# Kernel tuning notes

Hardware: AMD Instinct MI355X
Metric: run time of the kernel (lower is better)

## Reference

```python
import math
import jax, jax.numpy as jnp
import numpy as np

N = 100000      # nodes
E = 800000      # edges (before self loops)
D_IN = 128      # dim_node
D_H = 64        # dim_hidden
N_CLS = 40      # num_classes
L = 4           # num_layers
ALPHA = 0.1
THETA = 0.5


def setup_inputs() -> dict:
    key = jax.random.key(0)
    ks = jax.random.split(key, 7)
    x = jax.random.normal(ks[0], (N, D_IN), dtype=jnp.float32)
    edge_index = jax.random.randint(ks[1], (2, E), 0, N, dtype=jnp.int64)
    fc0_w = jax.random.normal(ks[2], (D_IN, D_H), dtype=jnp.float32) / math.sqrt(D_IN)
    fc0_b = jnp.zeros((D_H,), dtype=jnp.float32)
    fc1_w = jax.random.normal(ks[3], (D_H, N_CLS), dtype=jnp.float32) / math.sqrt(D_H)
    fc1_b = jnp.zeros((N_CLS,), dtype=jnp.float32)
    conv_w = jax.random.normal(ks[4], (L, D_H, D_H), dtype=jnp.float32) / math.sqrt(D_H)
    return {"x": x, "edge_index": edge_index, "fc0_w": fc0_w, "fc0_b": fc0_b,
            "fc1_w": fc1_w, "fc1_b": fc1_b, "conv_w": conv_w}


def reference(x, edge_index, fc0_w, fc0_b, fc1_w, fc1_b, conv_w):
    # gcn_norm with add_self_loops=True, improved=False (fill_value=1)
    self_idx = jnp.arange(N, dtype=edge_index.dtype)
    row = jnp.concatenate([edge_index[0], self_idx])   # source
    col = jnp.concatenate([edge_index[1], self_idx])   # target
    w = jnp.ones((E + N,), dtype=x.dtype)
    deg = jax.ops.segment_sum(w, col, num_segments=N)
    dinv = jnp.where(deg > 0, jax.lax.rsqrt(deg), 0.0)
    norm = dinv[row] * w * dinv[col]                   # [E+N]

    def prop(h):
        # gather + edge-weight scale + scatter-add (GCNII propagate)
        return jax.ops.segment_sum(norm[:, None] * h[row], col, num_segments=N)

    # fc0 + relu (dropout is identity in eval)
    h = jax.nn.relu(x @ fc0_w + fc0_b)
    # first conv: x_0 is None -> just propagate, then relu
    h = jax.nn.relu(prop(h))
    x0 = h
    for i in range(1, L):
        beta = math.log(THETA / (i + 1) + 1.0)
        m = prop(h)
        m = (1.0 - ALPHA) * m + ALPHA * x0
        # addmm(m, m, W1, beta=1-beta, alpha=beta)
        h = jax.nn.relu((1.0 - beta) * m + beta * (m @ conv_w[i]))
    return h @ fc1_w + fc1_b
```

## Files before the change

### kernel.cpp

```cpp
#include <hip/hip_runtime.h>
#include <hip/hip_fp16.h>

#define N_NODES 100000
#define N_EDGES 800000
#define N_BUCKET 391
#define L_HIST (N_BUCKET * 256)

__device__ inline float4 f4zero() { return make_float4(0.f, 0.f, 0.f, 0.f); }

__device__ inline unsigned pack2u(float a, float b) {
    union { unsigned u; __half2 h; } r; r.h = __floats2half2_rn(a, b); return r.u;
}
__device__ inline float2 unpack2f(unsigned u) {
    union { unsigned uu; __half2 h; } d; d.uu = u; return __half22float2(d.h);
}

typedef _Float16 hf2 __attribute__((ext_vector_type(2)));
__device__ inline float fdot2(unsigned a, unsigned b, float c) {
#if __has_builtin(__builtin_amdgcn_fdot2)
    union { unsigned u; hf2 h; } ua, ub; ua.u = a; ub.u = b;
    return __builtin_amdgcn_fdot2(ua.h, ub.h, c, false);
#else
    float2 fa = unpack2f(a), fb = unpack2f(b);
    return fmaf(fa.x, fb.x, fmaf(fa.y, fb.y, c));
#endif
}

__device__ inline uint4 pack8(const float f[8]) {
    uint4 u;
    u.x = pack2u(f[0], f[1]); u.y = pack2u(f[2], f[3]);
    u.z = pack2u(f[4], f[5]); u.w = pack2u(f[6], f[7]);
    return u;
}
__device__ inline void unpack8(uint4 u, float f[8]) {
    float2 t;
    t = unpack2f(u.x); f[0] = t.x; f[1] = t.y;
    t = unpack2f(u.y); f[2] = t.x; f[3] = t.y;
    t = unpack2f(u.z); f[4] = t.x; f[5] = t.y;
    t = unpack2f(u.w); f[6] = t.x; f[7] = t.y;
}


__global__ __launch_bounds__(256) void k_hist(const int* __restrict__ col, int* __restrict__ histT) {
    __shared__ int hist[N_BUCKET];
    int b = blockIdx.x, t = threadIdx.x;
    for (int i = t; i < N_BUCKET; i += 256) hist[i] = 0;
    __syncthreads();
    const int base = b * 3125;
    for (int i = t; i < 3125; i += 256) atomicAdd(&hist[col[base + i] >> 8], 1);
    __syncthreads();
    for (int d = t; d < N_BUCKET; d += 256) histT[d * 256 + b] = hist[d];
}

__global__ __launch_bounds__(256) void k_scanA(const int* __restrict__ in, int* __restrict__ out,
                                               int* __restrict__ bsum, int L) {
    __shared__ int sh[256];
    int t = threadIdx.x, b = blockIdx.x;
    int base = b * 1024 + t * 4;
    int c0 = 0, c1 = 0, c2 = 0, c3 = 0;
    if (base + 3 < L) {
        int4 v = *reinterpret_cast<const int4*>(in + base);
        c0 = v.x; c1 = v.y; c2 = v.z; c3 = v.w;
    } else {
        if (base + 0 < L) c0 = in[base + 0];
        if (base + 1 < L) c1 = in[base + 1];
        if (base + 2 < L) c2 = in[base + 2];
    }
    int s = c0 + c1 + c2 + c3;
    sh[t] = s;
    __syncthreads();
    for (int off = 1; off < 256; off <<= 1) {
        int add = (t >= off) ? sh[t - off] : 0;
        __syncthreads();
        sh[t] += add;
        __syncthreads();
    }
    int excl = sh[t] - s;
    if (t == 255) bsum[b] = sh[t];
    int p = excl;
    if (base + 0 < L) out[base + 0] = p; p += c0;
    if (base + 1 < L) out[base + 1] = p; p += c1;
    if (base + 2 < L) out[base + 2] = p; p += c2;
    if (base + 3 < L) out[base + 3] = p;
}

__global__ __launch_bounds__(128) void k_scanB(int* __restrict__ bsum, int nb) {
    __shared__ int sh[128];
    int t = threadIdx.x;
    int v = (t < nb) ? bsum[t] : 0;
    sh[t] = v;
    __syncthreads();
    for (int off = 1; off < 128; off <<= 1) {
        int add = (t >= off) ? sh[t - off] : 0;
        __syncthreads();
        sh[t] += add;
        __syncthreads();
    }
    if (t < nb) bsum[t] = sh[t] - v;
}

__global__ __launch_bounds__(256) void k_scanC(int* __restrict__ out, const int* __restrict__ bsum, int L) {
    int t = threadIdx.x, b = blockIdx.x;
    int off = bsum[b];
    int base = b * 1024 + t * 4;
#pragma unroll
    for (int j = 0; j < 4; ++j)
        if (base + j < L) out[base + j] += off;
}

__global__ __launch_bounds__(256) void k_scatter1(const int* __restrict__ row, const int* __restrict__ col,
                                                  const int* __restrict__ hoff, unsigned* __restrict__ tmp) {
    __shared__ int lcnt[N_BUCKET];
    int b = blockIdx.x, t = threadIdx.x;
    for (int d = t; d < N_BUCKET; d += 256) lcnt[d] = hoff[d * 256 + b];
    __syncthreads();
    const int base = b * 3125;
    for (int i = t; i < 3125; i += 256) {
        int c = col[base + i];
        int r = row[base + i];
        int p = atomicAdd(&lcnt[c >> 8], 1);
        tmp[p] = ((unsigned)(c & 255) << 17) | (unsigned)r;
    }
}

__global__ __launch_bounds__(256) void k_bucket(const unsigned* __restrict__ tmp, const int* __restrict__ hoff,
                                                int* __restrict__ starts, int* __restrict__ csr,
                                                float* __restrict__ dinv, float* __restrict__ rsq) {
    __shared__ int hist[256], sh[256], cur[256];
    int d = blockIdx.x, t = threadIdx.x;
    int s0 = hoff[d * 256];
    int s1 = (d < N_BUCKET - 1) ? hoff[(d + 1) * 256] : N_EDGES;
    int len = s1 - s0;
    hist[t] = 0;
    __syncthreads();
    for (int i = t; i < len; i += 256) atomicAdd(&hist[tmp[s0 + i] >> 17], 1);
    __syncthreads();
    int h = hist[t];
    sh[t] = h;
    __syncthreads();
    for (int off = 1; off < 256; off <<= 1) {
        int add = (t >= off) ? sh[t - off] : 0;
        __syncthreads();
        sh[t] += add;
        __syncthreads();
    }
    int excl = sh[t] - h;
    int colg = d * 256 + t;
    if (colg < N_NODES) {
        starts[colg] = s0 + excl;
        dinv[colg] = rsqrtf((float)h + 1.f);
        rsq[colg]  = sqrtf((float)h + 1.f);
    }
    if (d == N_BUCKET - 1 && t == 0) starts[N_NODES] = N_EDGES;
    cur[t] = s0 + excl;
    __syncthreads();
    for (int i = t; i < len; i += 256) {
        unsigned e = tmp[s0 + i];
        int p = atomicAdd(&cur[e >> 17], 1);
        csr[p] = (int)(e & 0x1FFFFu);
    }
}

__global__ __launch_bounds__(256) void k_wcvt(const float* __restrict__ conv_w, const float* __restrict__ fc1_w,
                                              const float* __restrict__ fc0_w,
                                              unsigned* __restrict__ wh, unsigned* __restrict__ w1h,
                                              unsigned* __restrict__ w0h) {
    int i = blockIdx.x * 256 + threadIdx.x;
    if (i < 3 * 2048) {
        int layer = i >> 11, rem = i & 2047, kp = rem >> 6, c = rem & 63;
        const float* wsrc = conv_w + (size_t)(layer + 1) * 4096;
        wh[i] = pack2u(wsrc[(2 * kp) * 64 + c], wsrc[(2 * kp + 1) * 64 + c]);
        return;
    }
    int j = i - 3 * 2048;
    if (j < 1280) {
        int kp = j / 40, c = j - kp * 40;
        w1h[j] = pack2u(fc1_w[(2 * kp) * 40 + c], fc1_w[(2 * kp + 1) * 40 + c]);
        return;
    }
    int t = j - 1280;
    if (t < 4096) {
        int kp = t >> 6, c = t & 63;
        w0h[t] = pack2u(fc0_w[(2 * kp) * 64 + c], fc0_w[(2 * kp + 1) * 64 + c]);
    }
}

__global__ __launch_bounds__(256, 4) void k_fc0(const float* __restrict__ x, const unsigned* __restrict__ w0h,
                                                const float* __restrict__ bias, const float* __restrict__ dinv,
                                                uint2* __restrict__ out) {
    __shared__ unsigned wsh[64 * 64];
    __shared__ unsigned xs2[64 * 65];
    const float4* x4 = reinterpret_cast<const float4*>(x);
    int tid = threadIdx.x;
    int base = blockIdx.x * 64;
#pragma unroll
    for (int i = 0; i < 4; ++i)
        reinterpret_cast<uint4*>(wsh)[tid + 256 * i] = reinterpret_cast<const uint4*>(w0h)[tid + 256 * i];
#pragma unroll
    for (int j = 0; j < 8; ++j) {
        int f = tid + 256 * j;
        int ln = f >> 5, c = f & 31;
        float4 v = (base + ln < N_NODES) ? x4[(size_t)(base + ln) * 32 + c] : f4zero();
        xs2[ln * 65 + 2 * c]     = pack2u(v.x, v.y);
        xs2[ln * 65 + 2 * c + 1] = pack2u(v.z, v.w);
    }
    __syncthreads();
    int q = tid & 15, lbase = (tid >> 4) * 4;
    float4 bv = reinterpret_cast<const float4*>(bias)[q];
    float a[4][4];
#pragma unroll
    for (int n = 0; n < 4; ++n) { a[n][0] = bv.x; a[n][1] = bv.y; a[n][2] = bv.z; a[n][3] = bv.w; }
#pragma unroll 4
    for (int kp = 0; kp < 64; ++kp) {
        unsigned xh0 = xs2[(lbase + 0) * 65 + kp];
        unsigned xh1 = xs2[(lbase + 1) * 65 + kp];
        unsigned xh2 = xs2[(lbase + 2) * 65 + kp];
        unsigned xh3 = xs2[(lbase + 3) * 65 + kp];
        uint4 wv = *reinterpret_cast<const uint4*>(&wsh[kp * 64 + q * 4]);
        a[0][0] = fdot2(xh0, wv.x, a[0][0]); a[0][1] = fdot2(xh0, wv.y, a[0][1]);
        a[0][2] = fdot2(xh0, wv.z, a[0][2]); a[0][3] = fdot2(xh0, wv.w, a[0][3]);
        a[1][0] = fdot2(xh1, wv.x, a[1][0]); a[1][1] = fdot2(xh1, wv.y, a[1][1]);
        a[1][2] = fdot2(xh1, wv.z, a[1][2]); a[1][3] = fdot2(xh1, wv.w, a[1][3]);
        a[2][0] = fdot2(xh2, wv.x, a[2][0]); a[2][1] = fdot2(xh2, wv.y, a[2][1]);
        a[2][2] = fdot2(xh2, wv.z, a[2][2]); a[2][3] = fdot2(xh2, wv.w, a[2][3]);
        a[3][0] = fdot2(xh3, wv.x, a[3][0]); a[3][1] = fdot2(xh3, wv.y, a[3][1]);
        a[3][2] = fdot2(xh3, wv.z, a[3][2]); a[3][3] = fdot2(xh3, wv.w, a[3][3]);
    }
#pragma unroll
    for (int n = 0; n < 4; ++n) {
        int nn = base + lbase + n;
        if (nn < N_NODES) {
            float dc = dinv[nn];
            float r0 = dc * fmaxf(a[n][0], 0.f), r1 = dc * fmaxf(a[n][1], 0.f);
            float r2 = dc * fmaxf(a[n][2], 0.f), r3 = dc * fmaxf(a[n][3], 0.f);
            uint2 u; u.x = pack2u(r0, r1); u.y = pack2u(r2, r3);
            out[(size_t)nn * 16 + q] = u;
        }
    }
}

__device__ __forceinline__ void gather8h(const uint4* __restrict__ hp, const int* __restrict__ csr,
                                         int s, int e, int q, __half2 acc2[4]) {
    if (s >= e) return;
    int l = e - 1;
    int idx[8];
#pragma unroll
    for (int j = 0; j < 8; ++j) idx[j] = csr[min(s + j, l)];
    for (int p = s; p < e; p += 8) {
        uint4 d[8];
        unsigned msk[8];
#pragma unroll
        for (int j = 0; j < 8; ++j) {
            d[j] = hp[(size_t)idx[j] * 8 + q];
            msk[j] = (p + j <= l) ? 0x3C003C00u : 0u;
        }
        if (p + 8 < e) {
#pragma unroll
            for (int j = 0; j < 8; ++j) idx[j] = csr[min(p + 8 + j, l)];
        }
#pragma unroll
        for (int j = 0; j < 8; ++j) {
            __half2 w2 = *reinterpret_cast<__half2*>(&msk[j]);
            const __half2* h2 = reinterpret_cast<const __half2*>(&d[j]);
            acc2[0] = __hfma2(w2, h2[0], acc2[0]);
            acc2[1] = __hfma2(w2, h2[1], acc2[1]);
            acc2[2] = __hfma2(w2, h2[2], acc2[2]);
            acc2[3] = __hfma2(w2, h2[3], acc2[3]);
        }
    }
}

__global__ __launch_bounds__(256, 6) void k_prop0(const uint4* __restrict__ hp, uint4* __restrict__ x0p,
                                                  const float* __restrict__ dinv,
                                                  const int* __restrict__ starts, const int* __restrict__ csr) {
    int t = blockIdx.x * 256 + threadIdx.x;
    int node = t >> 3, q = t & 7;
    uint4 self = hp[(size_t)node * 8 + q];
    __half2 acc2[4];
    const __half2* sh2 = reinterpret_cast<const __half2*>(&self);
#pragma unroll
    for (int k = 0; k < 4; ++k) acc2[k] = sh2[k];
    gather8h(hp, csr, starts[node], starts[node + 1], q, acc2);
    float dc = dinv[node];
    float accf[8];
    unpack8(*reinterpret_cast<uint4*>(acc2), accf);
    float o[8];
#pragma unroll
    for (int k = 0; k < 8; ++k) o[k] = dc * fmaxf(dc * accf[k], 0.f);
    x0p[(size_t)node * 8 + q] = pack8(o);
}

template <bool FINAL>
__global__ __launch_bounds__(256, 6) void k_propconv(
    const uint4* __restrict__ hp_in, const uint4* __restrict__ x0p,
    const float* __restrict__ dinv, const float* __restrict__ rsq,
    const int* __restrict__ starts, const int* __restrict__ csr,
    const unsigned* __restrict__ wh, float beta,
    const unsigned* __restrict__ w1h, const float* __restrict__ b1,
    void* __restrict__ out) {
    __shared__ unsigned ws2[32 * 64];
    __shared__ unsigned ws12[FINAL ? 32 * 40 : 1];

    int tid = threadIdx.x;
    int nl = tid >> 3, q = tid & 7;
    int node = blockIdx.x * 32 + nl;

    reinterpret_cast<uint4*>(ws2)[tid]       = reinterpret_cast<const uint4*>(wh)[tid];
    reinterpret_cast<uint4*>(ws2)[tid + 256] = reinterpret_cast<const uint4*>(wh)[tid + 256];
    if constexpr (FINAL) {
        reinterpret_cast<uint4*>(ws12)[tid < 320 ? tid : 0] = reinterpret_cast<const uint4*>(w1h)[tid < 320 ? tid : 0];
        if (tid < 64) reinterpret_cast<uint4*>(ws12)[tid + 256] = reinterpret_cast<const uint4*>(w1h)[tid + 256];
    }

    uint4 self = hp_in[(size_t)node * 8 + q];
    __half2 acc2[4];
    const __half2* sh2 = reinterpret_cast<const __half2*>(&self);
#pragma unroll
    for (int k = 0; k < 4; ++k) acc2[k] = sh2[k];
    gather8h(hp_in, csr, starts[node], starts[node + 1], q, acc2);

    float dc = dinv[node];
    float rs = rsq[node];
    float accf[8], xq[8];
    unpack8(*reinterpret_cast<uint4*>(acc2), accf);
    unpack8(x0p[(size_t)node * 8 + q], xq);
    float m[8];
#pragma unroll
    for (int k = 0; k < 8; ++k) m[k] = 0.9f * dc * accf[k] + 0.1f * rs * xq[k];
    unsigned mh[4];
#pragma unroll
    for (int t = 0; t < 4; ++t) mh[t] = pack2u(m[2 * t], m[2 * t + 1]);

    __syncthreads();

    float a[8] = {0.f, 0.f, 0.f, 0.f, 0.f, 0.f, 0.f, 0.f};
#pragma unroll
    for (int src = 0; src < 8; ++src) {
        unsigned mm[4];
#pragma unroll
        for (int t = 0; t < 4; ++t) mm[t] = (unsigned)__shfl((int)mh[t], src, 8);
#pragma unroll
        for (int t = 0; t < 4; ++t) {
            int kp = src * 4 + t;
            const uint4* wr = reinterpret_cast<const uint4*>(&ws2[kp * 64 + q * 8]);
            uint4 w0 = wr[0], w1 = wr[1];
            a[0] = fdot2(mm[t], w0.x, a[0]); a[1] = fdot2(mm[t], w0.y, a[1]);
            a[2] = fdot2(mm[t], w0.z, a[2]); a[3] = fdot2(mm[t], w0.w, a[3]);
            a[4] = fdot2(mm[t], w1.x, a[4]); a[5] = fdot2(mm[t], w1.y, a[5]);
            a[6] = fdot2(mm[t], w1.z, a[6]); a[7] = fdot2(mm[t], w1.w, a[7]);
        }
    }
    float omb = 1.f - beta;
    float r[8];
#pragma unroll
    for (int k = 0; k < 8; ++k) r[k] = fmaxf(fmaf(omb, m[k], beta * a[k]), 0.f);

    if constexpr (!FINAL) {
        float o[8];
#pragma unroll
        for (int k = 0; k < 8; ++k) o[k] = dc * r[k];
        reinterpret_cast<uint4*>(out)[(size_t)node * 8 + q] = pack8(o);
    } else {
        unsigned rh[4];
#pragma unroll
        for (int t = 0; t < 4; ++t) rh[t] = pack2u(r[2 * t], r[2 * t + 1]);
        float acc1[5];
#pragma unroll
        for (int j = 0; j < 5; ++j) acc1[j] = b1[q * 5 + j];
#pragma unroll
        for (int src = 0; src < 8; ++src) {
            unsigned rm[4];
#pragma unroll
            for (int t = 0; t < 4; ++t) rm[t] = (unsigned)__shfl((int)rh[t], src, 8);
#pragma unroll
            for (int t = 0; t < 4; ++t) {
                int kp = src * 4 + t;
                const unsigned* wr = &ws12[kp * 40 + q * 5];
#pragma unroll
                for (int j = 0; j < 5; ++j) acc1[j] = fdot2(rm[t], wr[j], acc1[j]);
            }
        }
        float* o = reinterpret_cast<float*>(out) + (size_t)node * 40 + q * 5;
#pragma unroll
        for (int j = 0; j < 5; ++j) o[j] = acc1[j];
    }
}


extern "C" void kernel_launch(void* const* d_in, const int* in_sizes, int n_in,
                              void* d_out, int out_size, void* d_ws, size_t ws_size,
                              hipStream_t stream) {
    const float* x      = (const float*)d_in[0];
    const int*   ei     = (const int*)d_in[1];
    const float* fc0_w  = (const float*)d_in[2];
    const float* fc0_b  = (const float*)d_in[3];
    const float* fc1_w  = (const float*)d_in[4];
    const float* fc1_b  = (const float*)d_in[5];
    const float* conv_w = (const float*)d_in[6];
    const int* row = ei;
    const int* col = ei + N_EDGES;

    char* ws = (char*)d_ws;
    size_t off = 0;
    auto alloc = [&](size_t bytes) -> void* {
        void* p = ws + off;
        off += (bytes + 255) & ~(size_t)255;
        return p;
    };
    float*    dinv   = (float*)alloc((size_t)N_NODES * 4);
    float*    rsq    = (float*)alloc((size_t)N_NODES * 4);
    int*      starts = (int*)alloc((size_t)(N_NODES + 1) * 4);
    int*      histT  = (int*)alloc((size_t)L_HIST * 4);
    int*      hoff   = (int*)alloc((size_t)L_HIST * 4);
    int*      bsum   = (int*)alloc(128 * 4);
    unsigned* tmp    = (unsigned*)alloc((size_t)N_EDGES * 4);
    int*      csr    = (int*)alloc((size_t)N_EDGES * 4);
    unsigned* wh     = (unsigned*)alloc(3 * 2048 * 4);
    unsigned* w1h    = (unsigned*)alloc(1280 * 4);
    unsigned* w0h    = (unsigned*)alloc(4096 * 4);
    uint4*    hp0    = (uint4*)alloc((size_t)N_NODES * 128);
    uint4*    x0p    = (uint4*)alloc((size_t)N_NODES * 128);
    uint4*    hpA    = (uint4*)alloc((size_t)N_NODES * 128);
    uint4*    hpB    = (uint4*)alloc((size_t)N_NODES * 128);
    if (off > ws_size) return;

    const int NBH = (L_HIST + 1023) / 1024;
    const int GMM = (N_NODES + 63) / 64;
    const int GP  = (N_NODES * 8) / 256;
    const int GPC = N_NODES / 32;

    k_wcvt<<<45, 256, 0, stream>>>(conv_w, fc1_w, fc0_w, wh, w1h, w0h);
    k_hist<<<256, 256, 0, stream>>>(col, histT);
    k_scanA<<<NBH, 256, 0, stream>>>(histT, hoff, bsum, L_HIST);
    k_scanB<<<1, 128, 0, stream>>>(bsum, NBH);
    k_scanC<<<NBH, 256, 0, stream>>>(hoff, bsum, L_HIST);
    k_scatter1<<<256, 256, 0, stream>>>(row, col, hoff, tmp);
    k_bucket<<<N_BUCKET, 256, 0, stream>>>(tmp, hoff, starts, csr, dinv, rsq);

    k_fc0<<<GMM, 256, 0, stream>>>(x, w0h, fc0_b, dinv, (uint2*)hp0);
    k_prop0<<<GP, 256, 0, stream>>>(hp0, x0p, dinv, starts, csr);

    const float betas[4] = {0.f, logf(0.5f / 2.f + 1.f), logf(0.5f / 3.f + 1.f), logf(0.5f / 4.f + 1.f)};

    k_propconv<false><<<GPC, 256, 0, stream>>>(x0p, x0p, dinv, rsq, starts, csr,
                                               wh + 0 * 2048, betas[1], nullptr, nullptr, hpA);
    k_propconv<false><<<GPC, 256, 0, stream>>>(hpA, x0p, dinv, rsq, starts, csr,
                                               wh + 1 * 2048, betas[2], nullptr, nullptr, hpB);
    k_propconv<true><<<GPC, 256, 0, stream>>>(hpB, x0p, dinv, rsq, starts, csr,
                                              wh + 2 * 2048, betas[3], w1h, fc1_b, d_out);
}
```

Before: 158.0 us.

## Reorder nodes by in-degree so gather warps see balanced neighbor counts

Adds a counting sort of nodes by in-degree, builds perm and inverse-perm tables, relabels CSR neighbor indices and stores per-node metadata (start, degree, dinv, rsq) in permuted order. The fc0 output is scattered into permuted positions and the final layer writes back through perm. The aim is to cut wavefront divergence in the degree-dependent gather loops, since neighboring threads now get similar edge counts. In exchange it adds seven small preprocessing launches plus a full pass over the CSR, and permuting nodes may reduce locality of the gathered rows.

After: 181.4 us. 14.8% more time.

```diff
diff --git a/kernel.cpp b/kernel.cpp
--- a/kernel.cpp
+++ b/kernel.cpp
@@ -5,6 +5,8 @@
 #define N_EDGES 800000
 #define N_BUCKET 391
 #define L_HIST (N_BUCKET * 256)
+#define DBINS 64
+#define L_DH (DBINS * N_BUCKET)
 
 __device__ inline float4 f4zero() { return make_float4(0.f, 0.f, 0.f, 0.f); }
 
@@ -125,6 +127,7 @@
 
 __global__ __launch_bounds__(256) void k_bucket(const unsigned* __restrict__ tmp, const int* __restrict__ hoff,
                                                 int* __restrict__ starts, int* __restrict__ csr,
+                                                int* __restrict__ deg,
                                                 float* __restrict__ dinv, float* __restrict__ rsq) {
     __shared__ int hist[256], sh[256], cur[256];
     int d = blockIdx.x, t = threadIdx.x;
@@ -148,10 +151,10 @@
     int colg = d * 256 + t;
     if (colg < N_NODES) {
         starts[colg] = s0 + excl;
+        deg[colg] = h;
         dinv[colg] = rsqrtf((float)h + 1.f);
         rsq[colg]  = sqrtf((float)h + 1.f);
     }
-    if (d == N_BUCKET - 1 && t == 0) starts[N_NODES] = N_EDGES;
     cur[t] = s0 + excl;
     __syncthreads();
     for (int i = t; i < len; i += 256) {
@@ -159,6 +162,50 @@
         int p = atomicAdd(&cur[e >> 17], 1);
         csr[p] = (int)(e & 0x1FFFFu);
     }
+}
+
+
+__global__ __launch_bounds__(256) void k_dhist(const int* __restrict__ deg, int* __restrict__ dhT) {
+    __shared__ int h[DBINS];
+    int b = blockIdx.x, t = threadIdx.x;
+    if (t < DBINS) h[t] = 0;
+    __syncthreads();
+    int i = b * 256 + t;
+    if (i < N_NODES) atomicAdd(&h[min(deg[i], DBINS - 1)], 1);
+    __syncthreads();
+    if (t < DBINS) dhT[t * N_BUCKET + b] = h[t];
+}
+
+__global__ __launch_bounds__(256) void k_dscat(const int* __restrict__ deg, const int* __restrict__ dhoff,
+                                               int* __restrict__ perm) {
+    __shared__ int cur[DBINS];
+    int b = blockIdx.x, t = threadIdx.x;
+    if (t < DBINS) cur[t] = dhoff[t * N_BUCKET + b];
+    __syncthreads();
+    int i = b * 256 + t;
+    if (i < N_NODES) {
+        int p = atomicAdd(&cur[min(deg[i], DBINS - 1)], 1);
+        perm[p] = i;
+    }
+}
+
+__global__ __launch_bounds__(256) void k_pmeta(const int* __restrict__ perm, const int* __restrict__ starts,
+                                               const int* __restrict__ deg, const float* __restrict__ dinv,
+                                               const float* __restrict__ rsq,
+                                               int* __restrict__ invp, int2* __restrict__ pse,
+                                               float* __restrict__ pdinv, float* __restrict__ prsq) {
+    int g = blockIdx.x * 256 + threadIdx.x;
+    if (g >= N_NODES) return;
+    int n = perm[g];
+    invp[n] = g;
+    pse[g] = make_int2(starts[n], deg[n]);
+    pdinv[g] = dinv[n];
+    prsq[g] = rsq[n];
+}
+
+__global__ __launch_bounds__(256) void k_relab(int* __restrict__ csr, const int* __restrict__ invp) {
+    int i = blockIdx.x * 256 + threadIdx.x;
+    if (i < N_EDGES) csr[i] = invp[csr[i]];
 }
 
 __global__ __launch_bounds__(256) void k_wcvt(const float* __restrict__ conv_w, const float* __restrict__ fc1_w,
@@ -187,7 +234,7 @@
 
 __global__ __launch_bounds__(256, 4) void k_fc0(const float* __restrict__ x, const unsigned* __restrict__ w0h,
                                                 const float* __restrict__ bias, const float* __restrict__ dinv,
-                                                uint2* __restrict__ out) {
+                                                const int* __restrict__ invp, uint2* __restrict__ out) {
     __shared__ unsigned wsh[64 * 64];
     __shared__ unsigned xs2[64 * 65];
     const float4* x4 = reinterpret_cast<const float4*>(x);
@@ -231,10 +278,11 @@
         int nn = base + lbase + n;
         if (nn < N_NODES) {
             float dc = dinv[nn];
+            int pn = invp[nn];
             float r0 = dc * fmaxf(a[n][0], 0.f), r1 = dc * fmaxf(a[n][1], 0.f);
             float r2 = dc * fmaxf(a[n][2], 0.f), r3 = dc * fmaxf(a[n][3], 0.f);
             uint2 u; u.x = pack2u(r0, r1); u.y = pack2u(r2, r3);
-            out[(size_t)nn * 16 + q] = u;
+            out[(size_t)pn * 16 + q] = u;
         }
     }
 }
@@ -271,30 +319,32 @@
 }
 
 __global__ __launch_bounds__(256, 6) void k_prop0(const uint4* __restrict__ hp, uint4* __restrict__ x0p,
-                                                  const float* __restrict__ dinv,
-                                                  const int* __restrict__ starts, const int* __restrict__ csr) {
+                                                  const float* __restrict__ pdinv,
+                                                  const int2* __restrict__ pse, const int* __restrict__ csr) {
     int t = blockIdx.x * 256 + threadIdx.x;
-    int node = t >> 3, q = t & 7;
-    uint4 self = hp[(size_t)node * 8 + q];
+    int g = t >> 3, q = t & 7;
+    uint4 self = hp[(size_t)g * 8 + q];
     __half2 acc2[4];
     const __half2* sh2 = reinterpret_cast<const __half2*>(&self);
 #pragma unroll
     for (int k = 0; k < 4; ++k) acc2[k] = sh2[k];
-    gather8h(hp, csr, starts[node], starts[node + 1], q, acc2);
-    float dc = dinv[node];
+    int2 se = pse[g];
+    gather8h(hp, csr, se.x, se.x + se.y, q, acc2);
+    float dc = pdinv[g];
     float accf[8];
     unpack8(*reinterpret_cast<uint4*>(acc2), accf);
     float o[8];
 #pragma unroll
     for (int k = 0; k < 8; ++k) o[k] = dc * fmaxf(dc * accf[k], 0.f);
-    x0p[(size_t)node * 8 + q] = pack8(o);
+    x0p[(size_t)g * 8 + q] = pack8(o);
 }
 
 template <bool FINAL>
 __global__ __launch_bounds__(256, 6) void k_propconv(
     const uint4* __restrict__ hp_in, const uint4* __restrict__ x0p,
-    const float* __restrict__ dinv, const float* __restrict__ rsq,
-    const int* __restrict__ starts, const int* __restrict__ csr,
+    const float* __restrict__ pdinv, const float* __restrict__ prsq,
+    const int2* __restrict__ pse, const int* __restrict__ csr,
+    const int* __restrict__ perm,
     const unsigned* __restrict__ wh, float beta,
     const unsigned* __restrict__ w1h, const float* __restrict__ b1,
     void* __restrict__ out) {
@@ -303,7 +353,7 @@
 
     int tid = threadIdx.x;
     int nl = tid >> 3, q = tid & 7;
-    int node = blockIdx.x * 32 + nl;
+    int g = blockIdx.x * 32 + nl;
 
     reinterpret_cast<uint4*>(ws2)[tid]       = reinterpret_cast<const uint4*>(wh)[tid];
     reinterpret_cast<uint4*>(ws2)[tid + 256] = reinterpret_cast<const uint4*>(wh)[tid + 256];
@@ -312,18 +362,19 @@
         if (tid < 64) reinterpret_cast<uint4*>(ws12)[tid + 256] = reinterpret_cast<const uint4*>(w1h)[tid + 256];
     }
 
-    uint4 self = hp_in[(size_t)node * 8 + q];
+    uint4 self = hp_in[(size_t)g * 8 + q];
     __half2 acc2[4];
     const __half2* sh2 = reinterpret_cast<const __half2*>(&self);
 #pragma unroll
     for (int k = 0; k < 4; ++k) acc2[k] = sh2[k];
-    gather8h(hp_in, csr, starts[node], starts[node + 1], q, acc2);
-
-    float dc = dinv[node];
-    float rs = rsq[node];
+    int2 se = pse[g];
+    gather8h(hp_in, csr, se.x, se.x + se.y, q, acc2);
+
+    float dc = pdinv[g];
+    float rs = prsq[g];
     float accf[8], xq[8];
     unpack8(*reinterpret_cast<uint4*>(acc2), accf);
-    unpack8(x0p[(size_t)node * 8 + q], xq);
+    unpack8(x0p[(size_t)g * 8 + q], xq);
     float m[8];
 #pragma unroll
     for (int k = 0; k < 8; ++k) m[k] = 0.9f * dc * accf[k] + 0.1f * rs * xq[k];
@@ -359,7 +410,7 @@
         float o[8];
 #pragma unroll
         for (int k = 0; k < 8; ++k) o[k] = dc * r[k];
-        reinterpret_cast<uint4*>(out)[(size_t)node * 8 + q] = pack8(o);
+        reinterpret_cast<uint4*>(out)[(size_t)g * 8 + q] = pack8(o);
     } else {
         unsigned rh[4];
 #pragma unroll
@@ -380,7 +431,8 @@
                 for (int j = 0; j < 5; ++j) acc1[j] = fdot2(rm[t], wr[j], acc1[j]);
             }
         }
-        float* o = reinterpret_cast<float*>(out) + (size_t)node * 40 + q * 5;
+        int norig = perm[g];
+        float* o = reinterpret_cast<float*>(out) + (size_t)norig * 40 + q * 5;
 #pragma unroll
         for (int j = 0; j < 5; ++j) o[j] = acc1[j];
     }
@@ -409,12 +461,21 @@
     };
     float*    dinv   = (float*)alloc((size_t)N_NODES * 4);
     float*    rsq    = (float*)alloc((size_t)N_NODES * 4);
-    int*      starts = (int*)alloc((size_t)(N_NODES + 1) * 4);
+    int*      starts = (int*)alloc((size_t)N_NODES * 4);
+    int*      deg    = (int*)alloc((size_t)N_NODES * 4);
     int*      histT  = (int*)alloc((size_t)L_HIST * 4);
     int*      hoff   = (int*)alloc((size_t)L_HIST * 4);
-    int*      bsum   = (int*)alloc(128 * 4);
+    int*      bsumA  = (int*)alloc(128 * 4);
+    int*      bsumB  = (int*)alloc(128 * 4);
     unsigned* tmp    = (unsigned*)alloc((size_t)N_EDGES * 4);
     int*      csr    = (int*)alloc((size_t)N_EDGES * 4);
+    int*      dhT    = (int*)alloc((size_t)L_DH * 4);
+    int*      dhoff  = (int*)alloc((size_t)L_DH * 4);
+    int*      perm   = (int*)alloc((size_t)N_NODES * 4);
+    int*      invp   = (int*)alloc((size_t)N_NODES * 4);
+    int2*     pse    = (int2*)alloc((size_t)N_NODES * 8);
+    float*    pdinv  = (float*)alloc((size_t)N_NODES * 4);
+    float*    prsq   = (float*)alloc((size_t)N_NODES * 4);
     unsigned* wh     = (unsigned*)alloc(3 * 2048 * 4);
     unsigned* w1h    = (unsigned*)alloc(1280 * 4);
     unsigned* w0h    = (unsigned*)alloc(4096 * 4);
@@ -424,28 +485,37 @@
     uint4*    hpB    = (uint4*)alloc((size_t)N_NODES * 128);
     if (off > ws_size) return;
 
-    const int NBH = (L_HIST + 1023) / 1024;
-    const int GMM = (N_NODES + 63) / 64;
-    const int GP  = (N_NODES * 8) / 256;
-    const int GPC = N_NODES / 32;
+    const int NBH  = (L_HIST + 1023) / 1024;
+    const int NBD  = (L_DH + 1023) / 1024;
+    const int GMM  = (N_NODES + 63) / 64;
+    const int GP   = (N_NODES * 8) / 256;
+    const int GPC  = N_NODES / 32;
 
     k_wcvt<<<45, 256, 0, stream>>>(conv_w, fc1_w, fc0_w, wh, w1h, w0h);
     k_hist<<<256, 256, 0, stream>>>(col, histT);
-    k_scanA<<<NBH, 256, 0, stream>>>(histT, hoff, bsum, L_HIST);
-    k_scanB<<<1, 128, 0, stream>>>(bsum, NBH);
-    k_scanC<<<NBH, 256, 0, stream>>>(hoff, bsum, L_HIST);
+    k_scanA<<<NBH, 256, 0, stream>>>(histT, hoff, bsumA, L_HIST);
+    k_scanB<<<1, 128, 0, stream>>>(bsumA, NBH);
+    k_scanC<<<NBH, 256, 0, stream>>>(hoff, bsumA, L_HIST);
     k_scatter1<<<256, 256, 0, stream>>>(row, col, hoff, tmp);
-    k_bucket<<<N_BUCKET, 256, 0, stream>>>(tmp, hoff, starts, csr, dinv, rsq);
-
-    k_fc0<<<GMM, 256, 0, stream>>>(x, w0h, fc0_b, dinv, (uint2*)hp0);
-    k_prop0<<<GP, 256, 0, stream>>>(hp0, x0p, dinv, starts, csr);
+    k_bucket<<<N_BUCKET, 256, 0, stream>>>(tmp, hoff, starts, csr, deg, dinv, rsq);
+
+    k_dhist<<<N_BUCKET, 256, 0, stream>>>(deg, dhT);
+    k_scanA<<<NBD, 256, 0, stream>>>(dhT, dhoff, bsumB, L_DH);
+    k_scanB<<<1, 128, 0, stream>>>(bsumB, NBD);
+    k_scanC<<<NBD, 256, 0, stream>>>(dhoff, bsumB, L_DH);
+    k_dscat<<<N_BUCKET, 256, 0, stream>>>(deg, dhoff, perm);
+    k_pmeta<<<N_BUCKET, 256, 0, stream>>>(perm, starts, deg, dinv, rsq, invp, pse, pdinv, prsq);
+    k_relab<<<(N_EDGES + 255) / 256, 256, 0, stream>>>(csr, invp);
+
+    k_fc0<<<GMM, 256, 0, stream>>>(x, w0h, fc0_b, dinv, invp, (uint2*)hp0);
+    k_prop0<<<GP, 256, 0, stream>>>(hp0, x0p, pdinv, pse, csr);
 
     const float betas[4] = {0.f, logf(0.5f / 2.f + 1.f), logf(0.5f / 3.f + 1.f), logf(0.5f / 4.f + 1.f)};
 
-    k_propconv<false><<<GPC, 256, 0, stream>>>(x0p, x0p, dinv, rsq, starts, csr,
+    k_propconv<false><<<GPC, 256, 0, stream>>>(x0p, x0p, pdinv, prsq, pse, csr, perm,
                                                wh + 0 * 2048, betas[1], nullptr, nullptr, hpA);
-    k_propconv<false><<<GPC, 256, 0, stream>>>(hpA, x0p, dinv, rsq, starts, csr,
+    k_propconv<false><<<GPC, 256, 0, stream>>>(hpA, x0p, pdinv, prsq, pse, csr, perm,
                                                wh + 1 * 2048, betas[2], nullptr, nullptr, hpB);
-    k_propconv<true><<<GPC, 256, 0, stream>>>(hpB, x0p, dinv, rsq, starts, csr,
+    k_propconv<true><<<GPC, 256, 0, stream>>>(hpB, x0p, pdinv, prsq, pse, csr, perm,
                                               wh + 2 * 2048, betas[3], w1h, fc1_b, d_out);
 }
```
